# Kernel tuning notes

Measured on AMD Instinct MI355X. Metric: run time of the kernel, lower is better.

The kernel has to match this reference:

```python
import jax, jax.numpy as jnp
import numpy as np

UP = jnp.array([0.0, 1.0, 0.0], dtype=jnp.float32)
LEASH = 15.0


def q_inv(q):
    return jnp.concatenate([-q[..., :3], q[..., 3:]], axis=-1)


def q_mul(q1, q2):
    x1, y1, z1, w1 = q1[..., 0], q1[..., 1], q1[..., 2], q1[..., 3]
    x2, y2, z2, w2 = q2[..., 0], q2[..., 1], q2[..., 2], q2[..., 3]
    return jnp.stack([
        w1 * x2 + x1 * w2 + y1 * z2 - z1 * y2,
        w1 * y2 - x1 * z2 + y1 * w2 + z1 * x2,
        w1 * z2 + x1 * y2 - y1 * x2 + z1 * w2,
        w1 * w2 - x1 * x2 - y1 * y2 - z1 * z2], axis=-1)


def q_rot(q, v):
    qv, qw = q[..., :3], q[..., 3:]
    t = 2.0 * jnp.cross(qv, v)
    return v + qw * t + jnp.cross(qv, t)


def mat_to_quat(R):
    # Batched [E,3,3] -> [E,4] (x,y,z,w), matching the torch branch structure.
    r = lambda i, j: R[:, i, j]
    eps = 1e-12
    tr = r(0, 0) + r(1, 1) + r(2, 2)
    Sa = jnp.sqrt(jnp.maximum(tr + 1.0, eps)) * 2.0
    qa = jnp.stack([(r(2, 1) - r(1, 2)) / Sa, (r(0, 2) - r(2, 0)) / Sa,
                    (r(1, 0) - r(0, 1)) / Sa, 0.25 * Sa], -1)
    Sb = jnp.sqrt(jnp.maximum(1.0 + r(0, 0) - r(1, 1) - r(2, 2), eps)) * 2.0
    qb = jnp.stack([0.25 * Sb, (r(0, 1) + r(1, 0)) / Sb,
                    (r(0, 2) + r(2, 0)) / Sb, (r(2, 1) - r(1, 2)) / Sb], -1)
    Sc = jnp.sqrt(jnp.maximum(1.0 + r(1, 1) - r(0, 0) - r(2, 2), eps)) * 2.0
    qc = jnp.stack([(r(0, 1) + r(1, 0)) / Sc, 0.25 * Sc,
                    (r(1, 2) + r(2, 1)) / Sc, (r(0, 2) - r(2, 0)) / Sc], -1)
    Sd = jnp.sqrt(jnp.maximum(1.0 + r(2, 2) - r(0, 0) - r(1, 1), eps)) * 2.0
    qd = jnp.stack([(r(0, 2) + r(2, 0)) / Sd, (r(1, 2) + r(2, 1)) / Sd,
                    0.25 * Sd, (r(1, 0) - r(0, 1)) / Sd], -1)
    cond_b = ((r(0, 0) > r(1, 1)) & (r(0, 0) > r(2, 2)))[:, None]
    cond_c = (r(1, 1) > r(2, 2))[:, None]
    return jnp.where((tr > 0)[:, None], qa,
                     jnp.where(cond_b, qb, jnp.where(cond_c, qc, qd)))


def sfm_pose_loss(pred_t, pred_q, gt_t, gt_q, batch_counts):
    E = batch_counts.shape[0]
    N = pred_t.shape[0]
    counts = batch_counts.astype(jnp.float32)  # [E]
    seg = jnp.repeat(jnp.arange(E), batch_counts, total_repeat_length=N)  # [N]
    starts = jnp.cumsum(batch_counts) - batch_counts  # first index of each episode
    sseg = lambda x: jax.ops.segment_sum(x, seg, num_segments=E)

    # --- per-episode centering ---
    mu_p = sseg(pred_t) / counts[:, None]
    mu_g = sseg(gt_t) / counts[:, None]
    p_c = pred_t - mu_p[seg]
    g_c = gt_t - mu_g[seg]

    # degenerate episodes: too short or near-zero gt variance (unbiased var)
    g_var = sseg(jnp.sum(g_c ** 2, -1)) / (counts - 1.0)
    deg = (batch_counts < 4) | (g_var < 1e-4)  # [E]

    # --- Umeyama: batched 3x3 SVD of H = p_c^T @ g_c per episode ---
    H = sseg(p_c[:, :, None] * g_c[:, None, :])  # [E,3,3]
    H_safe = jnp.where(deg[:, None, None], jnp.diag(jnp.array([3.0, 2.0, 1.0])), H)
    U, S, Vh = jnp.linalg.svd(H_safe, full_matrices=False)
    V = jnp.swapaxes(Vh, -1, -2)
    R0 = jnp.einsum('eij,ekj->eik', V, U)  # V @ U^T
    sgn = jnp.where(jnp.linalg.det(R0) < 0, -1.0, 1.0)
    V_adj = V * jnp.stack([jnp.ones_like(sgn), jnp.ones_like(sgn), sgn], -1)[:, None, :]
    R = jnp.einsum('eij,ekj->eik', V_adj, U)  # [E,3,3]

    p_rot = jnp.einsum('nij,nj->ni', R[seg], p_c)
    denom = sseg(jnp.sum(p_c ** 2, -1))
    nom = sseg(jnp.sum(p_rot * g_c, -1))
    s = jnp.where(denom > 1e-6,
                  jnp.clip(nom / jnp.maximum(denom, 1e-6), 1e-3, 1e3), 1.0)

    # --- translation loss (per-episode mse, then mean over episodes) ---
    p_al = jnp.where(deg[seg][:, None], p_c, p_rot * s[seg][:, None])
    diff = p_al - g_c
    loss_trans = jnp.mean(sseg(jnp.sum(diff ** 2, -1)) / (counts * 3.0))

    # --- scale loss (only non-degenerate episodes) ---
    loss_scale = jnp.sum(jnp.where(deg, 0.0, jnp.log(jnp.abs(s) + 1e-6) ** 2)) / E

    # --- rotation loss ---
    q_align = mat_to_quat(R)  # [E,4]
    q0_p = pred_q[starts]
    q0_g = gt_q[starts]
    pq_deg = q_mul(q_inv(q0_p)[seg], pred_q)
    gq_deg = q_mul(q_inv(q0_g)[seg], gt_q)
    pq_ume = q_mul(q_align[seg], pred_q)
    dm = deg[seg][:, None]
    pq_al = jnp.where(dm, pq_deg, pq_ume)
    gq_al = jnp.where(dm, gq_deg, gt_q)
    dot = jnp.sum(pq_al * gq_al, -1)
    loss_rot = jnp.mean(sseg(1.0 - dot ** 2) / counts)

    # --- gravity loss ---
    up = jnp.broadcast_to(UP, pred_q.shape[:-1] + (3,))
    pu = q_rot(q_inv(pred_q), up)
    gu = q_rot(q_inv(gt_q), up)
    cos = jnp.sum(pu * gu, -1) / jnp.maximum(
        jnp.linalg.norm(pu, axis=-1) * jnp.linalg.norm(gu, axis=-1), 1e-8)
    loss_grav = jnp.mean(sseg(1.0 - cos) / counts)

    # --- frame0 leash (deadzone on first translation of each episode) ---
    mag = jnp.linalg.norm(pred_t[starts], axis=-1)
    loss_leash = jnp.mean(jnp.maximum(mag - LEASH, 0.0) ** 2)

    return jnp.stack([loss_trans, loss_rot, loss_grav, loss_leash, loss_scale])


def setup_inputs() -> dict:
    rng = np.random.default_rng(0)
    E = 4096
    counts = rng.integers(64, 449, size=E)
    counts[:8] = np.array([2, 3, 3, 2, 3, 2, 3, 3])  # exercise degenerate branch
    N = int(counts.sum())
    key = jax.random.key(0)
    k1, k2, k3, k4 = jax.random.split(key, 4)
    pred_t = jax.random.normal(k1, (N, 3), dtype=jnp.float32) * 5.0
    gt_t = jax.random.normal(k2, (N, 3), dtype=jnp.float32) * 5.0

    def rand_unit_quat(k):
        q = jax.random.normal(k, (N, 4), dtype=jnp.float32)
        return q / jnp.linalg.norm(q, axis=-1, keepdims=True)

    return {
        'pred_t': pred_t,
        'pred_q': rand_unit_quat(k3),
        'gt_t': gt_t,
        'gt_q': rand_unit_quat(k4),
        'batch_counts': jnp.asarray(counts, dtype=jnp.int32),
    }


def reference(pred_t, pred_q, gt_t, gt_q, batch_counts):
    # Returns [loss_trans, loss_rot, loss_grav, loss_leash, loss_scale]
    return sfm_pose_loss(pred_t, pred_q, gt_t, gt_q, batch_counts)
```

## Files before the change

kernel.cpp:

```cpp
#include <hip/hip_runtime.h>
#include <math.h>

#define NACC 29

__device__ __forceinline__ float4 qmul4(float4 a, float4 b) {
    return make_float4(
        a.w*b.x + a.x*b.w + a.y*b.z - a.z*b.y,
        a.w*b.y - a.x*b.z + a.y*b.w + a.z*b.x,
        a.w*b.z + a.x*b.y - a.y*b.x + a.z*b.w,
        a.w*b.w - a.x*b.x - a.y*b.y - a.z*b.z);
}

__device__ __forceinline__ void qinv_rot_up(float4 q, float out[3]) {
    float qx = -q.x, qy = -q.y, qz = -q.z, qw = q.w;
    float tx = -2.f*qz;
    float ty = 0.f;
    float tz = 2.f*qx;
    out[0] = 0.f + qw*tx + (qy*tz - qz*ty);
    out[1] = 1.f + qw*ty + (qz*tx - qx*tz);
    out[2] = 0.f + qw*tz + (qx*ty - qy*tx);
}

__global__ void scan_zero_kernel(const int* __restrict__ counts,
                                 int* __restrict__ starts,
                                 float* __restrict__ out, int E) {
    __shared__ int lds[1024];
    int tid = threadIdx.x;
    if (tid < 5) out[tid] = 0.0f;
    int base = tid * 4;
    int c0 = (base + 0 < E) ? counts[base + 0] : 0;
    int c1 = (base + 1 < E) ? counts[base + 1] : 0;
    int c2 = (base + 2 < E) ? counts[base + 2] : 0;
    int c3 = (base + 3 < E) ? counts[base + 3] : 0;
    lds[tid] = c0 + c1 + c2 + c3;
    __syncthreads();
    for (int off = 1; off < 1024; off <<= 1) {
        int v = lds[tid];
        int a = (tid >= off) ? lds[tid - off] : 0;
        __syncthreads();
        lds[tid] = v + a;
        __syncthreads();
    }
    int excl = (tid > 0) ? lds[tid - 1] : 0;
    if (base + 0 < E) starts[base + 0] = excl; excl += c0;
    if (base + 1 < E) starts[base + 1] = excl; excl += c1;
    if (base + 2 < E) starts[base + 2] = excl; excl += c2;
    if (base + 3 < E) starts[base + 3] = excl;
}

__global__ __launch_bounds__(256) void pass1_kernel(
    const float* __restrict__ pred_t, const float4* __restrict__ pred_q,
    const float* __restrict__ gt_t,   const float4* __restrict__ gt_q,
    const int* __restrict__ counts, const int* __restrict__ starts,
    float* __restrict__ segacc)
{
    int e = blockIdx.x;
    int start = starts[e];
    int c = counts[e];
    float4 q0p = pred_q[start];
    float4 q0g = gt_q[start];
    float4 q0pi = make_float4(-q0p.x, -q0p.y, -q0p.z, q0p.w);
    float4 q0gi = make_float4(-q0g.x, -q0g.y, -q0g.z, q0g.w);

    float acc[NACC];
    #pragma unroll
    for (int k = 0; k < NACC; ++k) acc[k] = 0.f;

    for (int i = threadIdx.x; i < c; i += 256) {
        int n = start + i;
        float px = pred_t[3*n+0], py = pred_t[3*n+1], pz = pred_t[3*n+2];
        float gx = gt_t[3*n+0],  gy = gt_t[3*n+1],  gz = gt_t[3*n+2];
        float4 pq = pred_q[n];
        float4 gq = gt_q[n];

        acc[0] += px; acc[1] += py; acc[2] += pz;
        acc[3] += gx; acc[4] += gy; acc[5] += gz;
        acc[6] += px*px + py*py + pz*pz;
        acc[7] += gx*gx + gy*gy + gz*gz;
        acc[8]  += px*gx; acc[9]  += px*gy; acc[10] += px*gz;
        acc[11] += py*gx; acc[12] += py*gy; acc[13] += py*gz;
        acc[14] += pz*gx; acc[15] += pz*gy; acc[16] += pz*gz;

        float mx =  pq.w*gq.x - pq.z*gq.y + pq.y*gq.z - pq.x*gq.w;
        float my =  pq.z*gq.x + pq.w*gq.y - pq.x*gq.z - pq.y*gq.w;
        float mz = -pq.y*gq.x + pq.x*gq.y + pq.w*gq.z - pq.z*gq.w;
        float mw =  pq.x*gq.x + pq.y*gq.y + pq.z*gq.z + pq.w*gq.w;
        acc[17] += mx*mx; acc[18] += mx*my; acc[19] += mx*mz; acc[20] += mx*mw;
        acc[21] += my*my; acc[22] += my*mz; acc[23] += my*mw;
        acc[24] += mz*mz; acc[25] += mz*mw; acc[26] += mw*mw;

        float pu[3], gu[3];
        qinv_rot_up(pq, pu);
        qinv_rot_up(gq, gu);
        float nn = sqrtf(pu[0]*pu[0]+pu[1]*pu[1]+pu[2]*pu[2]) *
                   sqrtf(gu[0]*gu[0]+gu[1]*gu[1]+gu[2]*gu[2]);
        float cosv = (pu[0]*gu[0]+pu[1]*gu[1]+pu[2]*gu[2]) / fmaxf(nn, 1e-8f);
        acc[27] += 1.f - cosv;

        float4 aa = qmul4(q0pi, pq);
        float4 bb = qmul4(q0gi, gq);
        float dd = aa.x*bb.x + aa.y*bb.y + aa.z*bb.z + aa.w*bb.w;
        acc[28] += 1.f - dd*dd;
    }

    #pragma unroll
    for (int k = 0; k < NACC; ++k) {
        float v = acc[k];
        v += __shfl_down(v, 32);
        v += __shfl_down(v, 16);
        v += __shfl_down(v, 8);
        v += __shfl_down(v, 4);
        v += __shfl_down(v, 2);
        v += __shfl_down(v, 1);
        acc[k] = v;
    }
    __shared__ float red[4][NACC];
    int lane = threadIdx.x & 63;
    int wv = threadIdx.x >> 6;
    if (lane == 0) {
        #pragma unroll
        for (int k = 0; k < NACC; ++k) red[wv][k] = acc[k];
    }
    __syncthreads();
    if (threadIdx.x < NACC) {
        float s = red[0][threadIdx.x] + red[1][threadIdx.x] +
                  red[2][threadIdx.x] + red[3][threadIdx.x];
        segacc[(size_t)e*32 + threadIdx.x] = s;
    }
}

__device__ void jacobi3(double A[3][3], double V[3][3]) {
    V[0][0]=1.0; V[0][1]=0.0; V[0][2]=0.0;
    V[1][0]=0.0; V[1][1]=1.0; V[1][2]=0.0;
    V[2][0]=0.0; V[2][1]=0.0; V[2][2]=1.0;
    for (int sweep = 0; sweep < 20; ++sweep) {
        double off = A[0][1]*A[0][1] + A[0][2]*A[0][2] + A[1][2]*A[1][2];
        double dia = A[0][0]*A[0][0] + A[1][1]*A[1][1] + A[2][2]*A[2][2];
        if (off <= 1e-28 * (dia + 1e-300)) break;
        for (int p = 0; p < 2; ++p) for (int q = p + 1; q < 3; ++q) {
            double apq = A[p][q];
            if (fabs(apq) < 1e-300) continue;
            double theta = (A[q][q] - A[p][p]) / (2.0 * apq);
            double t = ((theta >= 0.0) ? 1.0 : -1.0) / (fabs(theta) + sqrt(theta*theta + 1.0));
            double cc = 1.0 / sqrt(t*t + 1.0);
            double ss = t * cc;
            double app = A[p][p], aqq = A[q][q];
            A[p][p] = app - t * apq;
            A[q][q] = aqq + t * apq;
            A[p][q] = 0.0; A[q][p] = 0.0;
            int r = 3 - p - q;
            double arp = A[r][p], arq = A[r][q];
            A[r][p] = cc*arp - ss*arq; A[p][r] = A[r][p];
            A[r][q] = ss*arp + cc*arq; A[q][r] = A[r][q];
            for (int i = 0; i < 3; ++i) {
                double vip = V[i][p], viq = V[i][q];
                V[i][p] = cc*vip - ss*viq;
                V[i][q] = ss*vip + cc*viq;
            }
        }
    }
}

__device__ void mat2quat(const double R[3][3], double q[4]) {
    const double eps = 1e-12;
    double tr = R[0][0] + R[1][1] + R[2][2];
    if (tr > 0.0) {
        double S = sqrt(fmax(tr + 1.0, eps)) * 2.0;
        q[0] = (R[2][1]-R[1][2])/S; q[1] = (R[0][2]-R[2][0])/S;
        q[2] = (R[1][0]-R[0][1])/S; q[3] = 0.25*S;
    } else if ((R[0][0] > R[1][1]) && (R[0][0] > R[2][2])) {
        double S = sqrt(fmax(1.0 + R[0][0] - R[1][1] - R[2][2], eps)) * 2.0;
        q[0] = 0.25*S; q[1] = (R[0][1]+R[1][0])/S;
        q[2] = (R[0][2]+R[2][0])/S; q[3] = (R[2][1]-R[1][2])/S;
    } else if (R[1][1] > R[2][2]) {
        double S = sqrt(fmax(1.0 + R[1][1] - R[0][0] - R[2][2], eps)) * 2.0;
        q[0] = (R[0][1]+R[1][0])/S; q[1] = 0.25*S;
        q[2] = (R[1][2]+R[2][1])/S; q[3] = (R[0][2]-R[2][0])/S;
    } else {
        double S = sqrt(fmax(1.0 + R[2][2] - R[0][0] - R[1][1], eps)) * 2.0;
        q[0] = (R[0][2]+R[2][0])/S; q[1] = (R[1][2]+R[2][1])/S;
        q[2] = 0.25*S; q[3] = (R[1][0]-R[0][1])/S;
    }
}

__global__ __launch_bounds__(256) void finalize_kernel(
    const float* __restrict__ segacc, const int* __restrict__ counts,
    const int* __restrict__ starts, const float* __restrict__ pred_t,
    float* __restrict__ out, int E)
{
    int e = blockIdx.x * 256 + threadIdx.x;
    double v_trans = 0.0, v_rot = 0.0, v_grav = 0.0, v_leash = 0.0, v_scale = 0.0;
    if (e < E) {
        const float* A = segacc + (size_t)e * 32;
        int ci = counts[e];
        double c = (double)ci;
        double mu_p[3] = { A[0]/c, A[1]/c, A[2]/c };
        double mu_g[3] = { A[3]/c, A[4]/c, A[5]/c };
        double pp_c = (double)A[6] - c*(mu_p[0]*mu_p[0]+mu_p[1]*mu_p[1]+mu_p[2]*mu_p[2]);
        double gg_c = (double)A[7] - c*(mu_g[0]*mu_g[0]+mu_g[1]*mu_g[1]+mu_g[2]*mu_g[2]);
        double H[3][3];
        H[0][0]=(double)A[8] -c*mu_p[0]*mu_g[0]; H[0][1]=(double)A[9] -c*mu_p[0]*mu_g[1]; H[0][2]=(double)A[10]-c*mu_p[0]*mu_g[2];
        H[1][0]=(double)A[11]-c*mu_p[1]*mu_g[0]; H[1][1]=(double)A[12]-c*mu_p[1]*mu_g[1]; H[1][2]=(double)A[13]-c*mu_p[1]*mu_g[2];
        H[2][0]=(double)A[14]-c*mu_p[2]*mu_g[0]; H[2][1]=(double)A[15]-c*mu_p[2]*mu_g[1]; H[2][2]=(double)A[16]-c*mu_p[2]*mu_g[2];
        double g_var = gg_c / (c - 1.0);
        bool deg = (ci < 4) || (g_var < 1e-4);
        double trH = H[0][0] + H[1][1] + H[2][2];
        double trans, rot, scale = 0.0;
        if (deg) {
            trans = (pp_c - 2.0*trH + gg_c) / (c * 3.0);
            rot = (double)A[28] / c;
        } else {
            double B[3][3], V[3][3];
            for (int i = 0; i < 3; ++i)
                for (int j = 0; j < 3; ++j)
                    B[i][j] = H[0][i]*H[0][j] + H[1][i]*H[1][j] + H[2][i]*H[2][j];
            jacobi3(B, V);
            double lam[3] = { B[0][0], B[1][1], B[2][2] };
            int idx[3] = {0, 1, 2};
            if (lam[idx[0]] < lam[idx[1]]) { int t = idx[0]; idx[0] = idx[1]; idx[1] = t; }
            if (lam[idx[0]] < lam[idx[2]]) { int t = idx[0]; idx[0] = idx[2]; idx[2] = t; }
            if (lam[idx[1]] < lam[idx[2]]) { int t = idx[1]; idx[1] = idx[2]; idx[2] = t; }
            double v1[3], v2[3], v3[3];
            for (int i = 0; i < 3; ++i) { v1[i] = V[i][idx[0]]; v2[i] = V[i][idx[1]]; v3[i] = V[i][idx[2]]; }
            double detV = v1[0]*(v2[1]*v3[2]-v2[2]*v3[1])
                        - v1[1]*(v2[0]*v3[2]-v2[2]*v3[0])
                        + v1[2]*(v2[0]*v3[1]-v2[1]*v3[0]);
            double sgnV = (detV < 0.0) ? -1.0 : 1.0;
            double u1[3], u2[3], u3[3];
            for (int i = 0; i < 3; ++i) u1[i] = H[i][0]*v1[0] + H[i][1]*v1[1] + H[i][2]*v1[2];
            double n1 = sqrt(u1[0]*u1[0]+u1[1]*u1[1]+u1[2]*u1[2]);
            n1 = fmax(n1, 1e-30);
            for (int i = 0; i < 3; ++i) u1[i] /= n1;
            for (int i = 0; i < 3; ++i) u2[i] = H[i][0]*v2[0] + H[i][1]*v2[1] + H[i][2]*v2[2];
            double d12 = u1[0]*u2[0]+u1[1]*u2[1]+u1[2]*u2[2];
            for (int i = 0; i < 3; ++i) u2[i] -= d12*u1[i];
            double n2 = sqrt(u2[0]*u2[0]+u2[1]*u2[1]+u2[2]*u2[2]);
            n2 = fmax(n2, 1e-30);
            for (int i = 0; i < 3; ++i) u2[i] /= n2;
            u3[0] = u1[1]*u2[2] - u1[2]*u2[1];
            u3[1] = u1[2]*u2[0] - u1[0]*u2[2];
            u3[2] = u1[0]*u2[1] - u1[1]*u2[0];
            double R[3][3];
            for (int i = 0; i < 3; ++i)
                for (int k = 0; k < 3; ++k)
                    R[i][k] = v1[i]*u1[k] + v2[i]*u2[k] + sgnV*v3[i]*u3[k];
            double nom = 0.0;
            for (int k = 0; k < 3; ++k)
                for (int j = 0; j < 3; ++j)
                    nom += R[k][j] * H[j][k];
            double denom = pp_c;
            double s = 1.0;
            if (denom > 1e-6) {
                s = nom / fmax(denom, 1e-6);
                s = fmin(fmax(s, 1e-3), 1e3);
            }
            trans = (s*s*denom - 2.0*s*nom + gg_c) / (c * 3.0);
            double ls = log(fabs(s) + 1e-6);
            scale = ls * ls;
            double q[4];
            mat2quat(R, q);
            double M00=A[17], M01=A[18], M02=A[19], M03=A[20], M11=A[21],
                   M12=A[22], M13=A[23], M22=A[24], M23=A[25], M33=A[26];
            double quad = q[0]*q[0]*M00 + q[1]*q[1]*M11 + q[2]*q[2]*M22 + q[3]*q[3]*M33
                + 2.0*(q[0]*q[1]*M01 + q[0]*q[2]*M02 + q[0]*q[3]*M03
                     + q[1]*q[2]*M12 + q[1]*q[3]*M13 + q[2]*q[3]*M23);
            rot = (c - quad) / c;
        }
        double grav = (double)A[27] / c;
        int st = starts[e];
        double tx = (double)pred_t[3*st+0], ty = (double)pred_t[3*st+1], tz = (double)pred_t[3*st+2];
        double mag = sqrt(tx*tx + ty*ty + tz*tz);
        double ml = fmax(mag - 15.0, 0.0);
        double Ed = (double)E;
        v_trans = trans / Ed;
        v_rot   = rot / Ed;
        v_grav  = grav / Ed;
        v_leash = (ml * ml) / Ed;
        v_scale = scale / Ed;
    }
    __shared__ double sd[256];
    double vals[5] = { v_trans, v_rot, v_grav, v_leash, v_scale };
    for (int k = 0; k < 5; ++k) {
        sd[threadIdx.x] = vals[k];
        __syncthreads();
        for (int off = 128; off > 0; off >>= 1) {
            if (threadIdx.x < off) sd[threadIdx.x] += sd[threadIdx.x + off];
            __syncthreads();
        }
        if (threadIdx.x == 0) atomicAdd(out + k, (float)sd[0]);
        __syncthreads();
    }
}

extern "C" void kernel_launch(void* const* d_in, const int* in_sizes, int n_in,
                              void* d_out, int out_size, void* d_ws, size_t ws_size,
                              hipStream_t stream) {
    const float*  pred_t = (const float*)d_in[0];
    const float4* pred_q = (const float4*)d_in[1];
    const float*  gt_t   = (const float*)d_in[2];
    const float4* gt_q   = (const float4*)d_in[3];
    const int*    counts = (const int*)d_in[4];
    int E = in_sizes[4];

    int* starts = (int*)d_ws;
    size_t off = ((size_t)E * sizeof(int) + 255) & ~(size_t)255;
    float* segacc = (float*)((char*)d_ws + off);

    scan_zero_kernel<<<1, 1024, 0, stream>>>(counts, starts, (float*)d_out, E);
    pass1_kernel<<<E, 256, 0, stream>>>(pred_t, pred_q, gt_t, gt_q, counts, starts, segacc);
    finalize_kernel<<<(E + 255) / 256, 256, 0, stream>>>(segacc, counts, starts, pred_t,
                                                         (float*)d_out, E);
}
```

Measured before the change: 139.1 us.

## Use single-wave blocks and float32 finalize with wave-only reductions

The per-episode accumulation kernel now runs one 64-thread wavefront per episode. Its reduction uses xor shuffles with no shared memory or barrier. The finalize kernel moves from double to float math, caps Jacobi sweeps at 6, and uses 64-thread blocks with a shuffle reduction instead of a shared-memory tree. This aims to cut FP64 latency, which is slow on this GPU, and barrier overhead, at the cost of precision in the SVD and centered covariance terms and fewer threads per episode in the streaming pass.

```diff
diff --git a/kernel.cpp b/kernel.cpp
--- a/kernel.cpp
+++ b/kernel.cpp
@@ -48,7 +48,7 @@
     if (base + 3 < E) starts[base + 3] = excl;
 }
 
-__global__ __launch_bounds__(256) void pass1_kernel(
+__global__ __launch_bounds__(64) void pass1_kernel(
     const float* __restrict__ pred_t, const float4* __restrict__ pred_q,
     const float* __restrict__ gt_t,   const float4* __restrict__ gt_q,
     const int* __restrict__ counts, const int* __restrict__ starts,
@@ -66,7 +66,7 @@
     #pragma unroll
     for (int k = 0; k < NACC; ++k) acc[k] = 0.f;
 
-    for (int i = threadIdx.x; i < c; i += 256) {
+    for (int i = threadIdx.x; i < c; i += 64) {
         int n = start + i;
         float px = pred_t[3*n+0], py = pred_t[3*n+1], pz = pred_t[3*n+2];
         float gx = gt_t[3*n+0],  gy = gt_t[3*n+1],  gz = gt_t[3*n+2];
@@ -106,189 +106,182 @@
     #pragma unroll
     for (int k = 0; k < NACC; ++k) {
         float v = acc[k];
+        v += __shfl_xor(v, 32);
+        v += __shfl_xor(v, 16);
+        v += __shfl_xor(v, 8);
+        v += __shfl_xor(v, 4);
+        v += __shfl_xor(v, 2);
+        v += __shfl_xor(v, 1);
+        acc[k] = v;
+    }
+    float outv = 0.f;
+    #pragma unroll
+    for (int k = 0; k < NACC; ++k)
+        if ((int)threadIdx.x == k) outv = acc[k];
+    if (threadIdx.x < NACC)
+        segacc[(size_t)e*32 + threadIdx.x] = outv;
+}
+
+__device__ void jacobi3f(float A[3][3], float V[3][3]) {
+    V[0][0]=1.f; V[0][1]=0.f; V[0][2]=0.f;
+    V[1][0]=0.f; V[1][1]=1.f; V[1][2]=0.f;
+    V[2][0]=0.f; V[2][1]=0.f; V[2][2]=1.f;
+    for (int sweep = 0; sweep < 6; ++sweep) {
+        float off = A[0][1]*A[0][1] + A[0][2]*A[0][2] + A[1][2]*A[1][2];
+        float dia = A[0][0]*A[0][0] + A[1][1]*A[1][1] + A[2][2]*A[2][2];
+        if (off <= 1e-12f * (dia + 1e-30f)) break;
+        for (int p = 0; p < 2; ++p) for (int q = p + 1; q < 3; ++q) {
+            float apq = A[p][q];
+            if (fabsf(apq) < 1e-30f) continue;
+            float theta = (A[q][q] - A[p][p]) / (2.0f * apq);
+            float t = ((theta >= 0.f) ? 1.f : -1.f) / (fabsf(theta) + sqrtf(theta*theta + 1.f));
+            float cc = 1.f / sqrtf(t*t + 1.f);
+            float ss = t * cc;
+            float app = A[p][p], aqq = A[q][q];
+            A[p][p] = app - t * apq;
+            A[q][q] = aqq + t * apq;
+            A[p][q] = 0.f; A[q][p] = 0.f;
+            int r = 3 - p - q;
+            float arp = A[r][p], arq = A[r][q];
+            A[r][p] = cc*arp - ss*arq; A[p][r] = A[r][p];
+            A[r][q] = ss*arp + cc*arq; A[q][r] = A[r][q];
+            for (int i = 0; i < 3; ++i) {
+                float vip = V[i][p], viq = V[i][q];
+                V[i][p] = cc*vip - ss*viq;
+                V[i][q] = ss*vip + cc*viq;
+            }
+        }
+    }
+}
+
+__device__ void mat2quatf(const float R[3][3], float q[4]) {
+    const float eps = 1e-12f;
+    float tr = R[0][0] + R[1][1] + R[2][2];
+    if (tr > 0.f) {
+        float S = sqrtf(fmaxf(tr + 1.f, eps)) * 2.f;
+        q[0] = (R[2][1]-R[1][2])/S; q[1] = (R[0][2]-R[2][0])/S;
+        q[2] = (R[1][0]-R[0][1])/S; q[3] = 0.25f*S;
+    } else if ((R[0][0] > R[1][1]) && (R[0][0] > R[2][2])) {
+        float S = sqrtf(fmaxf(1.f + R[0][0] - R[1][1] - R[2][2], eps)) * 2.f;
+        q[0] = 0.25f*S; q[1] = (R[0][1]+R[1][0])/S;
+        q[2] = (R[0][2]+R[2][0])/S; q[3] = (R[2][1]-R[1][2])/S;
+    } else if (R[1][1] > R[2][2]) {
+        float S = sqrtf(fmaxf(1.f + R[1][1] - R[0][0] - R[2][2], eps)) * 2.f;
+        q[0] = (R[0][1]+R[1][0])/S; q[1] = 0.25f*S;
+        q[2] = (R[1][2]+R[2][1])/S; q[3] = (R[0][2]-R[2][0])/S;
+    } else {
+        float S = sqrtf(fmaxf(1.f + R[2][2] - R[0][0] - R[1][1], eps)) * 2.f;
+        q[0] = (R[0][2]+R[2][0])/S; q[1] = (R[1][2]+R[2][1])/S;
+        q[2] = 0.25f*S; q[3] = (R[1][0]-R[0][1])/S;
+    }
+}
+
+__global__ __launch_bounds__(64) void finalize_kernel(
+    const float* __restrict__ segacc, const int* __restrict__ counts,
+    const int* __restrict__ starts, const float* __restrict__ pred_t,
+    float* __restrict__ out, int E)
+{
+    int e = blockIdx.x * 64 + threadIdx.x;
+    float v_trans = 0.f, v_rot = 0.f, v_grav = 0.f, v_leash = 0.f, v_scale = 0.f;
+    if (e < E) {
+        const float* A = segacc + (size_t)e * 32;
+        int ci = counts[e];
+        float c = (float)ci;
+        float mu_p[3] = { A[0]/c, A[1]/c, A[2]/c };
+        float mu_g[3] = { A[3]/c, A[4]/c, A[5]/c };
+        float pp_c = A[6] - c*(mu_p[0]*mu_p[0]+mu_p[1]*mu_p[1]+mu_p[2]*mu_p[2]);
+        float gg_c = A[7] - c*(mu_g[0]*mu_g[0]+mu_g[1]*mu_g[1]+mu_g[2]*mu_g[2]);
+        float H[3][3];
+        H[0][0]=A[8] -c*mu_p[0]*mu_g[0]; H[0][1]=A[9] -c*mu_p[0]*mu_g[1]; H[0][2]=A[10]-c*mu_p[0]*mu_g[2];
+        H[1][0]=A[11]-c*mu_p[1]*mu_g[0]; H[1][1]=A[12]-c*mu_p[1]*mu_g[1]; H[1][2]=A[13]-c*mu_p[1]*mu_g[2];
+        H[2][0]=A[14]-c*mu_p[2]*mu_g[0]; H[2][1]=A[15]-c*mu_p[2]*mu_g[1]; H[2][2]=A[16]-c*mu_p[2]*mu_g[2];
+        float g_var = gg_c / (c - 1.0f);
+        bool deg = (ci < 4) || (g_var < 1e-4f);
+        float trH = H[0][0] + H[1][1] + H[2][2];
+        float trans, rot, scale = 0.f;
+        if (deg) {
+            trans = (pp_c - 2.f*trH + gg_c) / (c * 3.f);
+            rot = A[28] / c;
+        } else {
+            float B[3][3], V[3][3];
+            for (int i = 0; i < 3; ++i)
+                for (int j = 0; j < 3; ++j)
+                    B[i][j] = H[0][i]*H[0][j] + H[1][i]*H[1][j] + H[2][i]*H[2][j];
+            jacobi3f(B, V);
+            float lam[3] = { B[0][0], B[1][1], B[2][2] };
+            int idx[3] = {0, 1, 2};
+            if (lam[idx[0]] < lam[idx[1]]) { int t = idx[0]; idx[0] = idx[1]; idx[1] = t; }
+            if (lam[idx[0]] < lam[idx[2]]) { int t = idx[0]; idx[0] = idx[2]; idx[2] = t; }
+            if (lam[idx[1]] < lam[idx[2]]) { int t = idx[1]; idx[1] = idx[2]; idx[2] = t; }
+            float v1[3], v2[3], v3[3];
+            for (int i = 0; i < 3; ++i) { v1[i] = V[i][idx[0]]; v2[i] = V[i][idx[1]]; v3[i] = V[i][idx[2]]; }
+            float detV = v1[0]*(v2[1]*v3[2]-v2[2]*v3[1])
+                       - v1[1]*(v2[0]*v3[2]-v2[2]*v3[0])
+                       + v1[2]*(v2[0]*v3[1]-v2[1]*v3[0]);
+            float sgnV = (detV < 0.f) ? -1.f : 1.f;
+            float u1[3], u2[3], u3[3];
+            for (int i = 0; i < 3; ++i) u1[i] = H[i][0]*v1[0] + H[i][1]*v1[1] + H[i][2]*v1[2];
+            float n1 = sqrtf(u1[0]*u1[0]+u1[1]*u1[1]+u1[2]*u1[2]);
+            n1 = fmaxf(n1, 1e-30f);
+            for (int i = 0; i < 3; ++i) u1[i] /= n1;
+            for (int i = 0; i < 3; ++i) u2[i] = H[i][0]*v2[0] + H[i][1]*v2[1] + H[i][2]*v2[2];
+            float d12 = u1[0]*u2[0]+u1[1]*u2[1]+u1[2]*u2[2];
+            for (int i = 0; i < 3; ++i) u2[i] -= d12*u1[i];
+            float n2 = sqrtf(u2[0]*u2[0]+u2[1]*u2[1]+u2[2]*u2[2]);
+            n2 = fmaxf(n2, 1e-30f);
+            for (int i = 0; i < 3; ++i) u2[i] /= n2;
+            u3[0] = u1[1]*u2[2] - u1[2]*u2[1];
+            u3[1] = u1[2]*u2[0] - u1[0]*u2[2];
+            u3[2] = u1[0]*u2[1] - u1[1]*u2[0];
+            float R[3][3];
+            for (int i = 0; i < 3; ++i)
+                for (int k = 0; k < 3; ++k)
+                    R[i][k] = v1[i]*u1[k] + v2[i]*u2[k] + sgnV*v3[i]*u3[k];
+            float nom = 0.f;
+            for (int k = 0; k < 3; ++k)
+                for (int j = 0; j < 3; ++j)
+                    nom += R[k][j] * H[j][k];
+            float denom = pp_c;
+            float s = 1.f;
+            if (denom > 1e-6f) {
+                s = nom / fmaxf(denom, 1e-6f);
+                s = fminf(fmaxf(s, 1e-3f), 1e3f);
+            }
+            trans = (s*s*denom - 2.f*s*nom + gg_c) / (c * 3.f);
+            float ls = logf(fabsf(s) + 1e-6f);
+            scale = ls * ls;
+            float q[4];
+            mat2quatf(R, q);
+            float M00=A[17], M01=A[18], M02=A[19], M03=A[20], M11=A[21],
+                  M12=A[22], M13=A[23], M22=A[24], M23=A[25], M33=A[26];
+            float quad = q[0]*q[0]*M00 + q[1]*q[1]*M11 + q[2]*q[2]*M22 + q[3]*q[3]*M33
+                + 2.f*(q[0]*q[1]*M01 + q[0]*q[2]*M02 + q[0]*q[3]*M03
+                     + q[1]*q[2]*M12 + q[1]*q[3]*M13 + q[2]*q[3]*M23);
+            rot = (c - quad) / c;
+        }
+        float grav = A[27] / c;
+        int st = starts[e];
+        float tx = pred_t[3*st+0], ty = pred_t[3*st+1], tz = pred_t[3*st+2];
+        float mag = sqrtf(tx*tx + ty*ty + tz*tz);
+        float ml = fmaxf(mag - 15.f, 0.f);
+        float Ed = (float)E;
+        v_trans = trans / Ed;
+        v_rot   = rot / Ed;
+        v_grav  = grav / Ed;
+        v_leash = (ml * ml) / Ed;
+        v_scale = scale / Ed;
+    }
+    float vals[5] = { v_trans, v_rot, v_grav, v_leash, v_scale };
+    #pragma unroll
+    for (int k = 0; k < 5; ++k) {
+        float v = vals[k];
         v += __shfl_down(v, 32);
         v += __shfl_down(v, 16);
         v += __shfl_down(v, 8);
         v += __shfl_down(v, 4);
         v += __shfl_down(v, 2);
         v += __shfl_down(v, 1);
-        acc[k] = v;
-    }
-    __shared__ float red[4][NACC];
-    int lane = threadIdx.x & 63;
-    int wv = threadIdx.x >> 6;
-    if (lane == 0) {
-        #pragma unroll
-        for (int k = 0; k < NACC; ++k) red[wv][k] = acc[k];
-    }
-    __syncthreads();
-    if (threadIdx.x < NACC) {
-        float s = red[0][threadIdx.x] + red[1][threadIdx.x] +
-                  red[2][threadIdx.x] + red[3][threadIdx.x];
-        segacc[(size_t)e*32 + threadIdx.x] = s;
-    }
-}
-
-__device__ void jacobi3(double A[3][3], double V[3][3]) {
-    V[0][0]=1.0; V[0][1]=0.0; V[0][2]=0.0;
-    V[1][0]=0.0; V[1][1]=1.0; V[1][2]=0.0;
-    V[2][0]=0.0; V[2][1]=0.0; V[2][2]=1.0;
-    for (int sweep = 0; sweep < 20; ++sweep) {
-        double off = A[0][1]*A[0][1] + A[0][2]*A[0][2] + A[1][2]*A[1][2];
-        double dia = A[0][0]*A[0][0] + A[1][1]*A[1][1] + A[2][2]*A[2][2];
-        if (off <= 1e-28 * (dia + 1e-300)) break;
-        for (int p = 0; p < 2; ++p) for (int q = p + 1; q < 3; ++q) {
-            double apq = A[p][q];
-            if (fabs(apq) < 1e-300) continue;
-            double theta = (A[q][q] - A[p][p]) / (2.0 * apq);
-            double t = ((theta >= 0.0) ? 1.0 : -1.0) / (fabs(theta) + sqrt(theta*theta + 1.0));
-            double cc = 1.0 / sqrt(t*t + 1.0);
-            double ss = t * cc;
-            double app = A[p][p], aqq = A[q][q];
-            A[p][p] = app - t * apq;
-            A[q][q] = aqq + t * apq;
-            A[p][q] = 0.0; A[q][p] = 0.0;
-            int r = 3 - p - q;
-            double arp = A[r][p], arq = A[r][q];
-            A[r][p] = cc*arp - ss*arq; A[p][r] = A[r][p];
-            A[r][q] = ss*arp + cc*arq; A[q][r] = A[r][q];
-            for (int i = 0; i < 3; ++i) {
-                double vip = V[i][p], viq = V[i][q];
-                V[i][p] = cc*vip - ss*viq;
-                V[i][q] = ss*vip + cc*viq;
-            }
-        }
-    }
-}
-
-__device__ void mat2quat(const double R[3][3], double q[4]) {
-    const double eps = 1e-12;
-    double tr = R[0][0] + R[1][1] + R[2][2];
-    if (tr > 0.0) {
-        double S = sqrt(fmax(tr + 1.0, eps)) * 2.0;
-        q[0] = (R[2][1]-R[1][2])/S; q[1] = (R[0][2]-R[2][0])/S;
-        q[2] = (R[1][0]-R[0][1])/S; q[3] = 0.25*S;
-    } else if ((R[0][0] > R[1][1]) && (R[0][0] > R[2][2])) {
-        double S = sqrt(fmax(1.0 + R[0][0] - R[1][1] - R[2][2], eps)) * 2.0;
-        q[0] = 0.25*S; q[1] = (R[0][1]+R[1][0])/S;
-        q[2] = (R[0][2]+R[2][0])/S; q[3] = (R[2][1]-R[1][2])/S;
-    } else if (R[1][1] > R[2][2]) {
-        double S = sqrt(fmax(1.0 + R[1][1] - R[0][0] - R[2][2], eps)) * 2.0;
-        q[0] = (R[0][1]+R[1][0])/S; q[1] = 0.25*S;
-        q[2] = (R[1][2]+R[2][1])/S; q[3] = (R[0][2]-R[2][0])/S;
-    } else {
-        double S = sqrt(fmax(1.0 + R[2][2] - R[0][0] - R[1][1], eps)) * 2.0;
-        q[0] = (R[0][2]+R[2][0])/S; q[1] = (R[1][2]+R[2][1])/S;
-        q[2] = 0.25*S; q[3] = (R[1][0]-R[0][1])/S;
-    }
-}
-
-__global__ __launch_bounds__(256) void finalize_kernel(
-    const float* __restrict__ segacc, const int* __restrict__ counts,
-    const int* __restrict__ starts, const float* __restrict__ pred_t,
-    float* __restrict__ out, int E)
-{
-    int e = blockIdx.x * 256 + threadIdx.x;
-    double v_trans = 0.0, v_rot = 0.0, v_grav = 0.0, v_leash = 0.0, v_scale = 0.0;
-    if (e < E) {
-        const float* A = segacc + (size_t)e * 32;
-        int ci = counts[e];
-        double c = (double)ci;
-        double mu_p[3] = { A[0]/c, A[1]/c, A[2]/c };
-        double mu_g[3] = { A[3]/c, A[4]/c, A[5]/c };
-        double pp_c = (double)A[6] - c*(mu_p[0]*mu_p[0]+mu_p[1]*mu_p[1]+mu_p[2]*mu_p[2]);
-        double gg_c = (double)A[7] - c*(mu_g[0]*mu_g[0]+mu_g[1]*mu_g[1]+mu_g[2]*mu_g[2]);
-        double H[3][3];
-        H[0][0]=(double)A[8] -c*mu_p[0]*mu_g[0]; H[0][1]=(double)A[9] -c*mu_p[0]*mu_g[1]; H[0][2]=(double)A[10]-c*mu_p[0]*mu_g[2];
-        H[1][0]=(double)A[11]-c*mu_p[1]*mu_g[0]; H[1][1]=(double)A[12]-c*mu_p[1]*mu_g[1]; H[1][2]=(double)A[13]-c*mu_p[1]*mu_g[2];
-        H[2][0]=(double)A[14]-c*mu_p[2]*mu_g[0]; H[2][1]=(double)A[15]-c*mu_p[2]*mu_g[1]; H[2][2]=(double)A[16]-c*mu_p[2]*mu_g[2];
-        double g_var = gg_c / (c - 1.0);
-        bool deg = (ci < 4) || (g_var < 1e-4);
-        double trH = H[0][0] + H[1][1] + H[2][2];
-        double trans, rot, scale = 0.0;
-        if (deg) {
-            trans = (pp_c - 2.0*trH + gg_c) / (c * 3.0);
-            rot = (double)A[28] / c;
-        } else {
-            double B[3][3], V[3][3];
-            for (int i = 0; i < 3; ++i)
-                for (int j = 0; j < 3; ++j)
-                    B[i][j] = H[0][i]*H[0][j] + H[1][i]*H[1][j] + H[2][i]*H[2][j];
-            jacobi3(B, V);
-            double lam[3] = { B[0][0], B[1][1], B[2][2] };
-            int idx[3] = {0, 1, 2};
-            if (lam[idx[0]] < lam[idx[1]]) { int t = idx[0]; idx[0] = idx[1]; idx[1] = t; }
-            if (lam[idx[0]] < lam[idx[2]]) { int t = idx[0]; idx[0] = idx[2]; idx[2] = t; }
-            if (lam[idx[1]] < lam[idx[2]]) { int t = idx[1]; idx[1] = idx[2]; idx[2] = t; }
-            double v1[3], v2[3], v3[3];
-            for (int i = 0; i < 3; ++i) { v1[i] = V[i][idx[0]]; v2[i] = V[i][idx[1]]; v3[i] = V[i][idx[2]]; }
-            double detV = v1[0]*(v2[1]*v3[2]-v2[2]*v3[1])
-                        - v1[1]*(v2[0]*v3[2]-v2[2]*v3[0])
-                        + v1[2]*(v2[0]*v3[1]-v2[1]*v3[0]);
-            double sgnV = (detV < 0.0) ? -1.0 : 1.0;
-            double u1[3], u2[3], u3[3];
-            for (int i = 0; i < 3; ++i) u1[i] = H[i][0]*v1[0] + H[i][1]*v1[1] + H[i][2]*v1[2];
-            double n1 = sqrt(u1[0]*u1[0]+u1[1]*u1[1]+u1[2]*u1[2]);
-            n1 = fmax(n1, 1e-30);
-            for (int i = 0; i < 3; ++i) u1[i] /= n1;
-            for (int i = 0; i < 3; ++i) u2[i] = H[i][0]*v2[0] + H[i][1]*v2[1] + H[i][2]*v2[2];
-            double d12 = u1[0]*u2[0]+u1[1]*u2[1]+u1[2]*u2[2];
-            for (int i = 0; i < 3; ++i) u2[i] -= d12*u1[i];
-            double n2 = sqrt(u2[0]*u2[0]+u2[1]*u2[1]+u2[2]*u2[2]);
-            n2 = fmax(n2, 1e-30);
-            for (int i = 0; i < 3; ++i) u2[i] /= n2;
-            u3[0] = u1[1]*u2[2] - u1[2]*u2[1];
-            u3[1] = u1[2]*u2[0] - u1[0]*u2[2];
-            u3[2] = u1[0]*u2[1] - u1[1]*u2[0];
-            double R[3][3];
-            for (int i = 0; i < 3; ++i)
-                for (int k = 0; k < 3; ++k)
-                    R[i][k] = v1[i]*u1[k] + v2[i]*u2[k] + sgnV*v3[i]*u3[k];
-            double nom = 0.0;
-            for (int k = 0; k < 3; ++k)
-                for (int j = 0; j < 3; ++j)
-                    nom += R[k][j] * H[j][k];
-            double denom = pp_c;
-            double s = 1.0;
-            if (denom > 1e-6) {
-                s = nom / fmax(denom, 1e-6);
-                s = fmin(fmax(s, 1e-3), 1e3);
-            }
-            trans = (s*s*denom - 2.0*s*nom + gg_c) / (c * 3.0);
-            double ls = log(fabs(s) + 1e-6);
-            scale = ls * ls;
-            double q[4];
-            mat2quat(R, q);
-            double M00=A[17], M01=A[18], M02=A[19], M03=A[20], M11=A[21],
-                   M12=A[22], M13=A[23], M22=A[24], M23=A[25], M33=A[26];
-            double quad = q[0]*q[0]*M00 + q[1]*q[1]*M11 + q[2]*q[2]*M22 + q[3]*q[3]*M33
-                + 2.0*(q[0]*q[1]*M01 + q[0]*q[2]*M02 + q[0]*q[3]*M03
-                     + q[1]*q[2]*M12 + q[1]*q[3]*M13 + q[2]*q[3]*M23);
-            rot = (c - quad) / c;
-        }
-        double grav = (double)A[27] / c;
-        int st = starts[e];
-        double tx = (double)pred_t[3*st+0], ty = (double)pred_t[3*st+1], tz = (double)pred_t[3*st+2];
-        double mag = sqrt(tx*tx + ty*ty + tz*tz);
-        double ml = fmax(mag - 15.0, 0.0);
-        double Ed = (double)E;
-        v_trans = trans / Ed;
-        v_rot   = rot / Ed;
-        v_grav  = grav / Ed;
-        v_leash = (ml * ml) / Ed;
-        v_scale = scale / Ed;
-    }
-    __shared__ double sd[256];
-    double vals[5] = { v_trans, v_rot, v_grav, v_leash, v_scale };
-    for (int k = 0; k < 5; ++k) {
-        sd[threadIdx.x] = vals[k];
-        __syncthreads();
-        for (int off = 128; off > 0; off >>= 1) {
-            if (threadIdx.x < off) sd[threadIdx.x] += sd[threadIdx.x + off];
-            __syncthreads();
-        }
-        if (threadIdx.x == 0) atomicAdd(out + k, (float)sd[0]);
-        __syncthreads();
+        if (threadIdx.x == 0) atomicAdd(out + k, v);
     }
 }
 
@@ -307,7 +300,7 @@
     float* segacc = (float*)((char*)d_ws + off);
 
     scan_zero_kernel<<<1, 1024, 0, stream>>>(counts, starts, (float*)d_out, E);
-    pass1_kernel<<<E, 256, 0, stream>>>(pred_t, pred_q, gt_t, gt_q, counts, starts, segacc);
-    finalize_kernel<<<(E + 255) / 256, 256, 0, stream>>>(segacc, counts, starts, pred_t,
-                                                         (float*)d_out, E);
-}
+    pass1_kernel<<<E, 64, 0, stream>>>(pred_t, pred_q, gt_t, gt_q, counts, starts, segacc);
+    finalize_kernel<<<(E + 63) / 64, 64, 0, stream>>>(segacc, counts, starts, pred_t,
+                                                      (float*)d_out, E);
+}
```

After: 121.8 us. 1.14x faster.
